# Performance work log

Measured on AMD Instinct MI355X. Metric: run time of the kernel, lower is better.

The kernel has to match this reference:

```python
import jax, jax.numpy as jnp
import numpy as np

NUM_TASKS, IN_SIZE, OUT_SIZE, N_ROWS = 64, 512, 512, 2048


def setup_inputs() -> dict:
    key = jax.random.key(0)
    k_x, k_t, k_w = jax.random.split(key, 3)
    inputs = jax.random.normal(k_x, (N_ROWS, IN_SIZE), dtype=jnp.float32)
    task_ids = jax.random.randint(k_t, (N_ROWS,), 0, NUM_TASKS, dtype=jnp.int64)
    # in_size == out_size path: identity + N(0, 0.03) perturbation per task
    W = (jnp.eye(IN_SIZE, OUT_SIZE, dtype=jnp.float32)[None]
         + 0.03 * jax.random.normal(k_w, (NUM_TASKS, IN_SIZE, OUT_SIZE), dtype=jnp.float32))
    return {"inputs": inputs, "task_ids": task_ids, "W": W}


def reference(inputs, task_ids, W):
    # Gather the full per-row weight matrix then batched vector-matrix multiply,
    # faithful to torch.einsum('ni,nio->no', inputs, W[task_ids]).
    aligned = W[task_ids]                       # [I, in, out]
    return jnp.einsum("ni,nio->no", inputs, aligned)  # [I, out]
```

## Files before the change

kernel.cpp:

```cpp
#include <hip/hip_runtime.h>


#define NDIM 512
#define KDIM 512
#define NCOL 32

typedef _Float16 f16x8 __attribute__((ext_vector_type(8)));
typedef float    f32x4 __attribute__((ext_vector_type(4)));

__global__ __launch_bounds__(256) void k_fused(
    const float* __restrict__ x,
    const int*   __restrict__ tids,
    const float* __restrict__ W,
    float*       __restrict__ out,
    int n_rows)
{
    const int tid  = threadIdx.x;
    const int lane = tid & 63;
    const int wv   = tid >> 6;
    const int c0   = blockIdx.x * NCOL;
    const int task = blockIdx.y;

    __shared__ __align__(16) _Float16 Wt[NCOL * KDIM];
    __shared__ unsigned short rlw[4 * 128];
    __shared__ unsigned short rl[256];
    __shared__ int wcnt[4];

    int trow[8], tval[8];
    #pragma unroll
    for (int it = 0; it < 8; ++it) {
        trow[it] = wv * 512 + it * 64 + lane;
        tval[it] = (trow[it] < n_rows) ? tids[trow[it]] : -1;
    }

    const int sc4   = (tid & 7) * 4;
    const int obase = tid >> 3;
    const float* Wg = W + (size_t)task * KDIM * NDIM + c0;
    float4 wr[16];
    #pragma unroll
    for (int j = 0; j < 8; ++j)
        wr[j] = *(const float4*)(Wg + (size_t)(obase * 8 + j) * NDIM + sc4);
    #pragma unroll
    for (int j = 0; j < 8; ++j)
        wr[8 + j] = *(const float4*)(Wg + (size_t)((obase + 32) * 8 + j) * NDIM + sc4);

    int cloc = 0;
    #pragma unroll
    for (int it = 0; it < 8; ++it) {
        const bool m = (tval[it] == task);
        const unsigned long long bal = __ballot(m);
        const int rank = __popcll(bal & ((1ull << lane) - 1ull));
        if (m) rlw[wv * 128 + cloc + rank] = (unsigned short)trow[it];
        cloc += __popcll(bal);
    }
    if (lane == 0) wcnt[wv] = cloc;

    #pragma unroll
    for (int h = 0; h < 2; ++h) {
        const int oct = obase + h * 32;
        #pragma unroll
        for (int j2 = 0; j2 < 4; ++j2) {
            f16x8 h8;
            #pragma unroll
            for (int j = 0; j < 8; ++j)
                h8[j] = (_Float16)(((const float*)&wr[h * 8 + j])[j2]);
            const int c  = sc4 + j2;
            const int po = oct ^ (c & 7);
            *(f16x8*)&Wt[c * KDIM + po * 8] = h8;
        }
    }

    __syncthreads();

    const int n0 = wcnt[0], n1 = wcnt[1], n2 = wcnt[2], n3 = wcnt[3];
    const int o1 = n0, o2 = n0 + n1, o3 = o2 + n2;
    const int count = o3 + n3;
    if (tid < count && tid < 256) {
        int w, base;
        if (tid < o1)      { w = 0; base = 0;  }
        else if (tid < o2) { w = 1; base = o1; }
        else if (tid < o3) { w = 2; base = o2; }
        else               { w = 3; base = o3; }
        rl[tid] = rlw[w * 128 + tid - base];
    }
    __syncthreads();

    if (count == 0) return;

    const int ml = lane & 15;
    const int q  = lane >> 4;

    for (int g0 = 0; g0 < count; g0 += 64) {
        const int rr = g0 + wv * 16 + ml;
        const int rowid = rl[(rr < count) ? rr : 0];
        const float* xrow = x + (size_t)rowid * KDIM;

        f32x4 acc[2] = {};
        #pragma unroll
        for (int p = 0; p < 2; ++p) {
            const int kb = p * 256;
            float4 xa[16];
            #pragma unroll
            for (int ks = 0; ks < 8; ++ks) {
                xa[2 * ks]     = *(const float4*)(xrow + kb + ks * 32 + q * 8);
                xa[2 * ks + 1] = *(const float4*)(xrow + kb + ks * 32 + q * 8 + 4);
            }
            #pragma unroll
            for (int ks = 0; ks < 8; ++ks) {
                f16x8 af;
                const float* a0 = (const float*)&xa[2 * ks];
                #pragma unroll
                for (int j = 0; j < 8; ++j) af[j] = (_Float16)a0[j];
                #pragma unroll
                for (int ct = 0; ct < 2; ++ct) {
                    const int cB = ct * 16 + ml;
                    const int po = (p * 32 + ks * 4 + q) ^ (cB & 7);
                    const f16x8 bf = *(const f16x8*)&Wt[cB * KDIM + po * 8];
                    acc[ct] = __builtin_amdgcn_mfma_f32_16x16x32_f16(af, bf, acc[ct], 0, 0, 0);
                }
            }
        }

        #pragma unroll
        for (int rg = 0; rg < 4; ++rg) {
            const int rr2 = g0 + wv * 16 + q * 4 + rg;
            if (rr2 < count) {
                float* op = out + (size_t)rl[rr2] * NDIM + c0 + ml;
                op[0]  = acc[0][rg];
                op[16] = acc[1][rg];
            }
        }
    }
}

extern "C" void kernel_launch(void* const* d_in, const int* in_sizes, int n_in,
                              void* d_out, int out_size, void* d_ws, size_t ws_size,
                              hipStream_t stream) {
    const float* x    = (const float*)d_in[0];
    const int*   tids = (const int*)d_in[1];
    const float* W    = (const float*)d_in[2];
    float*       out  = (float*)d_out;
    const int n_rows  = in_sizes[1];

    k_fused<<<dim3(NDIM / NCOL, 64), dim3(256), 0, stream>>>(x, tids, W, out, n_rows);
}
```

Baseline: 108.0 us.

## Stream weights directly from global memory per MFMA instead of staging in LDS

Column tile per block shrinks from 32 to 16, doubling the grid. The shared-memory fp16 weight tile and its swizzled transpose go away: each wave loads its B fragment straight from global memory with strided scalar loads and converts it in registers. The row-list buffers are enlarged so any per-task row count fits, and launch bounds request higher occupancy. The aim is to cut the LDS staging cost and raise occupancy, at the price of uncoalesced strided weight loads repeated by every wave and row group, and twice the scans of task ids.

```diff
diff --git a/kernel.cpp b/kernel.cpp
--- a/kernel.cpp
+++ b/kernel.cpp
@@ -3,12 +3,12 @@
 
 #define NDIM 512
 #define KDIM 512
-#define NCOL 32
+#define NCOL 16
 
 typedef _Float16 f16x8 __attribute__((ext_vector_type(8)));
 typedef float    f32x4 __attribute__((ext_vector_type(4)));
 
-__global__ __launch_bounds__(256) void k_fused(
+__global__ __launch_bounds__(256, 4) void k_fused(
     const float* __restrict__ x,
     const int*   __restrict__ tids,
     const float* __restrict__ W,
@@ -21,114 +21,73 @@
     const int c0   = blockIdx.x * NCOL;
     const int task = blockIdx.y;
 
-    __shared__ __align__(16) _Float16 Wt[NCOL * KDIM];
-    __shared__ unsigned short rlw[4 * 128];
-    __shared__ unsigned short rl[256];
+    __shared__ unsigned short rlw[4 * 512];
+    __shared__ unsigned short rl[2048];
     __shared__ int wcnt[4];
 
-    int trow[8], tval[8];
-    #pragma unroll
-    for (int it = 0; it < 8; ++it) {
-        trow[it] = wv * 512 + it * 64 + lane;
-        tval[it] = (trow[it] < n_rows) ? tids[trow[it]] : -1;
+    {
+        int cloc = 0;
+        #pragma unroll
+        for (int it = 0; it < 8; ++it) {
+            const int r = wv * 512 + it * 64 + lane;
+            const bool m = (r < n_rows) && (tids[r] == task);
+            const unsigned long long bal = __ballot(m);
+            const int rank = __popcll(bal & ((1ull << lane) - 1ull));
+            if (m) rlw[wv * 512 + cloc + rank] = (unsigned short)r;
+            cloc += __popcll(bal);
+        }
+        if (lane == 0) wcnt[wv] = cloc;
     }
-
-    const int sc4   = (tid & 7) * 4;
-    const int obase = tid >> 3;
-    const float* Wg = W + (size_t)task * KDIM * NDIM + c0;
-    float4 wr[16];
-    #pragma unroll
-    for (int j = 0; j < 8; ++j)
-        wr[j] = *(const float4*)(Wg + (size_t)(obase * 8 + j) * NDIM + sc4);
-    #pragma unroll
-    for (int j = 0; j < 8; ++j)
-        wr[8 + j] = *(const float4*)(Wg + (size_t)((obase + 32) * 8 + j) * NDIM + sc4);
-
-    int cloc = 0;
-    #pragma unroll
-    for (int it = 0; it < 8; ++it) {
-        const bool m = (tval[it] == task);
-        const unsigned long long bal = __ballot(m);
-        const int rank = __popcll(bal & ((1ull << lane) - 1ull));
-        if (m) rlw[wv * 128 + cloc + rank] = (unsigned short)trow[it];
-        cloc += __popcll(bal);
-    }
-    if (lane == 0) wcnt[wv] = cloc;
-
-    #pragma unroll
-    for (int h = 0; h < 2; ++h) {
-        const int oct = obase + h * 32;
-        #pragma unroll
-        for (int j2 = 0; j2 < 4; ++j2) {
-            f16x8 h8;
-            #pragma unroll
-            for (int j = 0; j < 8; ++j)
-                h8[j] = (_Float16)(((const float*)&wr[h * 8 + j])[j2]);
-            const int c  = sc4 + j2;
-            const int po = oct ^ (c & 7);
-            *(f16x8*)&Wt[c * KDIM + po * 8] = h8;
-        }
-    }
-
     __syncthreads();
-
-    const int n0 = wcnt[0], n1 = wcnt[1], n2 = wcnt[2], n3 = wcnt[3];
+    const int n0 = wcnt[0], n1 = wcnt[1], n2 = wcnt[2];
     const int o1 = n0, o2 = n0 + n1, o3 = o2 + n2;
-    const int count = o3 + n3;
-    if (tid < count && tid < 256) {
+    const int count = o3 + wcnt[3];
+    for (int i = tid; i < count; i += 256) {
         int w, base;
-        if (tid < o1)      { w = 0; base = 0;  }
-        else if (tid < o2) { w = 1; base = o1; }
-        else if (tid < o3) { w = 2; base = o2; }
-        else               { w = 3; base = o3; }
-        rl[tid] = rlw[w * 128 + tid - base];
+        if (i < o1)      { w = 0; base = 0;  }
+        else if (i < o2) { w = 1; base = o1; }
+        else if (i < o3) { w = 2; base = o2; }
+        else             { w = 3; base = o3; }
+        rl[i] = rlw[w * 512 + i - base];
     }
     __syncthreads();
 
-    if (count == 0) return;
-
     const int ml = lane & 15;
     const int q  = lane >> 4;
+    const float* Wg = W + (size_t)task * KDIM * NDIM + c0 + ml;
 
-    for (int g0 = 0; g0 < count; g0 += 64) {
-        const int rr = g0 + wv * 16 + ml;
-        const int rowid = rl[(rr < count) ? rr : 0];
-        const float* xrow = x + (size_t)rowid * KDIM;
+    for (int rg = wv; rg * 16 < count; rg += 4) {
+        const int rr = rg * 16 + ml;
+        const int rowm = rl[(rr < count) ? rr : 0];
+        const float* xrow = x + (size_t)rowm * KDIM + q * 8;
 
-        f32x4 acc[2] = {};
-        #pragma unroll
-        for (int p = 0; p < 2; ++p) {
-            const int kb = p * 256;
-            float4 xa[16];
+        f32x4 acc = {};
+        #pragma unroll 2
+        for (int kf = 0; kf < 16; ++kf) {
+            const int k0 = kf * 32;
+            const float* wp = Wg + (size_t)(k0 + q * 8) * NDIM;
+            float b[8];
             #pragma unroll
-            for (int ks = 0; ks < 8; ++ks) {
-                xa[2 * ks]     = *(const float4*)(xrow + kb + ks * 32 + q * 8);
-                xa[2 * ks + 1] = *(const float4*)(xrow + kb + ks * 32 + q * 8 + 4);
-            }
+            for (int j = 0; j < 8; ++j) b[j] = wp[(size_t)j * NDIM];
+            const float4 a0 = *(const float4*)(xrow + k0);
+            const float4 a1 = *(const float4*)(xrow + k0 + 4);
+
+            f16x8 af, bf;
+            af[0] = (_Float16)a0.x; af[1] = (_Float16)a0.y;
+            af[2] = (_Float16)a0.z; af[3] = (_Float16)a0.w;
+            af[4] = (_Float16)a1.x; af[5] = (_Float16)a1.y;
+            af[6] = (_Float16)a1.z; af[7] = (_Float16)a1.w;
             #pragma unroll
-            for (int ks = 0; ks < 8; ++ks) {
-                f16x8 af;
-                const float* a0 = (const float*)&xa[2 * ks];
-                #pragma unroll
-                for (int j = 0; j < 8; ++j) af[j] = (_Float16)a0[j];
-                #pragma unroll
-                for (int ct = 0; ct < 2; ++ct) {
-                    const int cB = ct * 16 + ml;
-                    const int po = (p * 32 + ks * 4 + q) ^ (cB & 7);
-                    const f16x8 bf = *(const f16x8*)&Wt[cB * KDIM + po * 8];
-                    acc[ct] = __builtin_amdgcn_mfma_f32_16x16x32_f16(af, bf, acc[ct], 0, 0, 0);
-                }
-            }
+            for (int j = 0; j < 8; ++j) bf[j] = (_Float16)b[j];
+
+            acc = __builtin_amdgcn_mfma_f32_16x16x32_f16(af, bf, acc, 0, 0, 0);
         }
 
         #pragma unroll
-        for (int rg = 0; rg < 4; ++rg) {
-            const int rr2 = g0 + wv * 16 + q * 4 + rg;
-            if (rr2 < count) {
-                float* op = out + (size_t)rl[rr2] * NDIM + c0 + ml;
-                op[0]  = acc[0][rg];
-                op[16] = acc[1][rg];
-            }
+        for (int rg2 = 0; rg2 < 4; ++rg2) {
+            const int rr2 = rg * 16 + q * 4 + rg2;
+            if (rr2 < count)
+                out[(size_t)rl[rr2] * NDIM + c0 + ml] = acc[rg2];
         }
     }
 }
```

New measurement: 131.6 us. 21.9% more time.
